# Optimization experiments

Hardware: AMD Instinct MI355X
Metric: run time of the kernel (lower is better)

Reference implementation:

```python
import jax, jax.numpy as jnp
import numpy as np

N_USERS, N_ITEMS, N_TOPICS = 200000, 100000, 100
N_NODES = N_USERS + N_ITEMS + N_TOPICS
N_EDGES = 5000000
DIM = 64
LAYERS = 3
BATCH = 16384


def setup_inputs() -> dict:
    key = jax.random.key(0)
    ks = jax.random.split(key, 8)
    users = jax.random.randint(ks[0], (BATCH,), 0, N_USERS, dtype=jnp.int64 if jax.config.jax_enable_x64 else jnp.int32)
    items = jax.random.randint(ks[1], (BATCH,), 0, N_ITEMS, dtype=jnp.int64 if jax.config.jax_enable_x64 else jnp.int32)
    edge_rows = jax.random.randint(ks[2], (N_EDGES,), 0, N_NODES, dtype=jnp.int32)
    edge_cols = jax.random.randint(ks[3], (N_EDGES,), 0, N_NODES, dtype=jnp.int32)
    # values ~ 1/deg to mimic the symmetric-normalized A_hat of LightGCN
    edge_vals = jax.random.uniform(ks[4], (N_EDGES,), dtype=jnp.float32) / 16.0
    user_emb = 0.1 * jax.random.normal(ks[5], (N_USERS, DIM), dtype=jnp.float32)
    item_emb = 0.1 * jax.random.normal(ks[6], (N_ITEMS, DIM), dtype=jnp.float32)
    topic_emb = 0.1 * jax.random.normal(ks[7], (N_TOPICS, DIM), dtype=jnp.float32)
    return {"users": users, "items": items, "edge_rows": edge_rows,
            "edge_cols": edge_cols, "edge_vals": edge_vals,
            "user_emb": user_emb, "item_emb": item_emb, "topic_emb": topic_emb}


def reference(users, items, edge_rows, edge_cols, edge_vals, user_emb, item_emb, topic_emb):
    n_users = user_emb.shape[0]
    n_nodes = n_users + item_emb.shape[0] + topic_emb.shape[0]
    # E^0 = [users; items; topics]
    h = jnp.concatenate([user_emb, item_emb, topic_emb], axis=0)  # [N, dim]
    acc = h
    for _ in range(LAYERS):
        # sparse A_hat @ h : gather source rows, scale by edge weight, scatter-add to dst
        msgs = edge_vals[:, None] * h[edge_cols]                  # [E, dim]
        h = jax.ops.segment_sum(msgs, edge_rows, num_segments=n_nodes)
        acc = acc + h
    out = acc / (LAYERS + 1)                                      # stack-mean over layers
    u = out[users]                                                # [B, dim]
    it = out[n_users + items]                                     # items offset into node table
    return jnp.sum(u * it, axis=1)                                # [B]
```

## Files before the change

kernel.cpp:

```cpp
#include <hip/hip_runtime.h>
#include <hip/hip_fp16.h>

#define N_USERS  200000
#define N_ITEMS  100000
#define N_TOPICS 100
#define N_NODES  (N_USERS + N_ITEMS + N_TOPICS)
#define DIM      64
#define BSHIFT   9
#define BROWS    (1 << BSHIFT)
#define NBUCKETS ((N_NODES + BROWS - 1) >> BSHIFT)
#define COLMASK  0x7FFFF
#define NB       512
#define NBSHIFT  9
#define M_TOT    (NBUCKETS * NB)
#define SB       256
#define CH       ((M_TOT + SB - 1) / SB)


__global__ void bucket_hist_kernel(const int* __restrict__ rows,
                                   int* __restrict__ partial, int n_edges) {
    __shared__ int h[NBUCKETS];
    for (int i = threadIdx.x; i < NBUCKETS; i += blockDim.x) h[i] = 0;
    __syncthreads();
    int stride = gridDim.x * blockDim.x;
    for (int e = blockIdx.x * blockDim.x + threadIdx.x; e < n_edges; e += stride)
        atomicAdd(&h[((unsigned)rows[e]) >> BSHIFT], 1);
    __syncthreads();
    for (int i = threadIdx.x; i < NBUCKETS; i += blockDim.x)
        partial[blockIdx.x * NBUCKETS + i] = h[i];
}

__device__ __forceinline__ int phys_idx(int L) {
    return (L & (NB - 1)) * NBUCKETS + (L >> NBSHIFT);
}

__global__ void scanB1_kernel(const int* __restrict__ partial,
                              int* __restrict__ psum) {
    __shared__ int s[256];
    int tid = threadIdx.x;
    int c0 = blockIdx.x * CH;
    int c1 = min(M_TOT, c0 + CH);
    int sum = 0;
    for (int L = c0 + tid; L < c1; L += 256) sum += partial[phys_idx(L)];
    s[tid] = sum;
    __syncthreads();
    for (int off = 128; off > 0; off >>= 1) {
        if (tid < off) s[tid] += s[tid + off];
        __syncthreads();
    }
    if (tid == 0) psum[blockIdx.x] = s[0];
}

__global__ void scanB2_kernel(int* __restrict__ psum) {
    __shared__ int s[SB];
    int tid = threadIdx.x;
    s[tid] = psum[tid];
    __syncthreads();
    for (int off = 1; off < SB; off <<= 1) {
        int v = (tid >= off) ? s[tid - off] : 0;
        __syncthreads();
        s[tid] += v;
        __syncthreads();
    }
    psum[tid] = tid ? s[tid - 1] : 0;
}

__global__ void scanB3_kernel(const int* __restrict__ partial,
                              const int* __restrict__ psum,
                              int* __restrict__ offs) {
    __shared__ int tile[256];
    __shared__ int carry;
    int tid = threadIdx.x;
    int c0 = blockIdx.x * CH;
    int c1 = min(M_TOT, c0 + CH);
    if (tid == 0) carry = psum[blockIdx.x];
    __syncthreads();
    for (int base = c0; base < c1; base += 256) {
        int L = base + tid;
        int v = (L < c1) ? partial[phys_idx(L)] : 0;
        tile[tid] = v;
        __syncthreads();
        for (int off = 1; off < 256; off <<= 1) {
            int t = (tid >= off) ? tile[tid - off] : 0;
            __syncthreads();
            tile[tid] += t;
            __syncthreads();
        }
        if (L < c1) offs[L] = carry + tile[tid] - v;
        __syncthreads();
        if (tid == 255) carry += tile[255];
        __syncthreads();
    }
}

__global__ void scatter1_kernel(const int* __restrict__ rows,
                                const int* __restrict__ cols,
                                const float* __restrict__ vals,
                                const int* __restrict__ offs,
                                int2* __restrict__ bkt_buf, int n_edges) {
    __shared__ int lpos[NBUCKETS];
    for (int i = threadIdx.x; i < NBUCKETS; i += blockDim.x)
        lpos[i] = offs[i * NB + blockIdx.x];
    __syncthreads();
    int stride = gridDim.x * blockDim.x;
    for (int e = blockIdx.x * blockDim.x + threadIdx.x; e < n_edges; e += stride) {
        int r = rows[e];
        int b = ((unsigned)r) >> BSHIFT;
        int pos = atomicAdd(&lpos[b], 1);
        int2 p;
        p.x = cols[e] | ((r & (BROWS - 1)) << 19);
        p.y = __float_as_int(vals[e]);
        bkt_buf[pos] = p;
    }
}

__global__ void scatter2_kernel(const int2* __restrict__ bkt_buf,
                                const int* __restrict__ offs,
                                int* __restrict__ row_ptr,
                                int2* __restrict__ csr_cv, int n_edges) {
    __shared__ int lcnt[BROWS];
    __shared__ int lptr[BROWS];
    __shared__ int lfill[BROWS];
    __shared__ int s[256];
    int b = blockIdx.x;
    int t = threadIdx.x;
    int e0 = offs[b * NB];
    int e1 = (b == NBUCKETS - 1) ? n_edges : offs[(b + 1) * NB];
    lcnt[t] = 0;          lcnt[t + 256] = 0;
    lfill[t] = 0;         lfill[t + 256] = 0;
    __syncthreads();
    for (int e = e0 + t; e < e1; e += blockDim.x)
        atomicAdd(&lcnt[((unsigned)bkt_buf[e].x) >> 19], 1);
    __syncthreads();
    s[t] = lcnt[2 * t] + lcnt[2 * t + 1];
    __syncthreads();
    for (int off = 1; off < 256; off <<= 1) {
        int v = (t >= off) ? s[t - off] : 0;
        __syncthreads();
        s[t] += v;
        __syncthreads();
    }
    int base = e0 + (t ? s[t - 1] : 0);
    int rbase = b << BSHIFT;
    int p_even = base;
    int p_odd  = base + lcnt[2 * t];
    lptr[2 * t]     = p_even;
    lptr[2 * t + 1] = p_odd;
    if (rbase + 2 * t     < N_NODES) row_ptr[rbase + 2 * t]     = p_even;
    if (rbase + 2 * t + 1 < N_NODES) row_ptr[rbase + 2 * t + 1] = p_odd;
    if (b == NBUCKETS - 1 && t == 0) row_ptr[N_NODES] = n_edges;
    __syncthreads();
    for (int e = e0 + t; e < e1; e += blockDim.x) {
        int2 p = bkt_buf[e];
        int delta = ((unsigned)p.x) >> 19;
        int pos = lptr[delta] + atomicAdd(&lfill[delta], 1);
        int2 cv;
        cv.x = p.x & COLMASK;
        cv.y = p.y;
        csr_cv[pos] = cv;
    }
}

__global__ void concat_f16_kernel(const float* __restrict__ uemb,
                                  const float* __restrict__ iemb,
                                  const float* __restrict__ temb,
                                  ushort* __restrict__ h0) {
    int g = blockIdx.x * blockDim.x + threadIdx.x;
    long base = (long)g * 4;
    if (base >= (long)N_NODES * DIM) return;
    const float* src;
    long off;
    if (base < (long)N_USERS * DIM)                 { src = uemb; off = base; }
    else if (base < (long)(N_USERS + N_ITEMS) * DIM){ src = iemb; off = base - (long)N_USERS * DIM; }
    else                                            { src = temb; off = base - (long)(N_USERS + N_ITEMS) * DIM; }
    float4 v = *(const float4*)(src + off);
    __half2 a = __floats2half2_rn(v.x, v.y);
    __half2 b = __floats2half2_rn(v.z, v.w);
    uint2 o;
    o.x = *(unsigned*)&a;
    o.y = *(unsigned*)&b;
    ((uint2*)h0)[g] = o;
}

__device__ __forceinline__ float4 fma_mix4(const ushort* __restrict__ h,
                                           int row, int l16, float w,
                                           float4 acc) {
    uint2 r = ((const uint2*)(h + (size_t)row * DIM))[l16];
    __half2 h01 = *(__half2*)&r.x;
    __half2 h23 = *(__half2*)&r.y;
    acc.x = __builtin_fmaf(__half2float(__low2half(h01)),  w, acc.x);
    acc.y = __builtin_fmaf(__half2float(__high2half(h01)), w, acc.y);
    acc.z = __builtin_fmaf(__half2float(__low2half(h23)),  w, acc.z);
    acc.w = __builtin_fmaf(__half2float(__high2half(h23)), w, acc.w);
    return acc;
}

__global__ void spmv_csr_kernel(const int* __restrict__ row_ptr,
                                const int2* __restrict__ csr_cv,
                                const ushort* __restrict__ h_src,
                                ushort* __restrict__ h_dst) {
    int wave = (int)(((long)blockIdx.x * blockDim.x + threadIdx.x) >> 6);
    int lane = threadIdx.x & 63;
    int g    = lane >> 4;
    int l16  = lane & 15;
    int r    = wave * 4 + g;
    int rc   = min(r, N_NODES - 1);
    int p0   = row_ptr[rc];
    int p1   = row_ptr[rc + 1];
    int len  = (r < N_NODES) ? (p1 - p0) : 0;
    int m = max(len, __shfl_xor(len, 16, 64));
    m = max(m, __shfl_xor(m, 32, 64));
    float4 acc = make_float4(0.f, 0.f, 0.f, 0.f);
    for (int off = 0; off < m; off += 8) {
        int2 cv[8];
        #pragma unroll
        for (int j = 0; j < 8; ++j) {
            bool k = (off + j) < len;
            cv[j] = csr_cv[k ? (p0 + off + j) : p0];
            if (!k) cv[j].y = 0;
        }
        #pragma unroll
        for (int j = 0; j < 8; ++j)
            acc = fma_mix4(h_src, cv[j].x, l16, __int_as_float(cv[j].y), acc);
    }
    if (r < N_NODES) {
        __half2 a = __floats2half2_rn(acc.x, acc.y);
        __half2 b = __floats2half2_rn(acc.z, acc.w);
        uint2 o;
        o.x = *(unsigned*)&a;
        o.y = *(unsigned*)&b;
        ((uint2*)(h_dst + (size_t)r * DIM))[l16] = o;
    }
}

__global__ void spmv_batch_kernel(const int* __restrict__ row_ptr,
                                  const int2* __restrict__ csr_cv,
                                  const ushort* __restrict__ h_src,
                                  const int* __restrict__ users,
                                  const int* __restrict__ items,
                                  float* __restrict__ u_acc,
                                  float* __restrict__ it_acc, int B) {
    int wave = (int)(((long)blockIdx.x * blockDim.x + threadIdx.x) >> 6);
    int lane = threadIdx.x & 63;
    int g    = lane >> 4;
    int l16  = lane & 15;
    int s    = wave * 4 + g;
    bool ok  = s < 2 * B;
    int node = 0;
    if (ok) node = (s < B) ? users[s] : (N_USERS + items[s - B]);
    int p0  = row_ptr[node];
    int p1  = row_ptr[node + 1];
    int len = ok ? (p1 - p0) : 0;
    int m = max(len, __shfl_xor(len, 16, 64));
    m = max(m, __shfl_xor(m, 32, 64));
    float4 acc = make_float4(0.f, 0.f, 0.f, 0.f);
    for (int off = 0; off < m; off += 8) {
        int2 cv[8];
        #pragma unroll
        for (int j = 0; j < 8; ++j) {
            bool k = (off + j) < len;
            cv[j] = csr_cv[k ? (p0 + off + j) : p0];
            if (!k) cv[j].y = 0;
        }
        #pragma unroll
        for (int j = 0; j < 8; ++j)
            acc = fma_mix4(h_src, cv[j].x, l16, __int_as_float(cv[j].y), acc);
    }
    if (ok) {
        float* dst = (s < B) ? (u_acc + (size_t)s * DIM)
                             : (it_acc + (size_t)(s - B) * DIM);
        float4* p = (float4*)dst + l16;
        float4 old = *p;
        old.x += acc.x; old.y += acc.y; old.z += acc.z; old.w += acc.w;
        *p = old;
    }
}


__global__ void gather_add_kernel(const ushort* __restrict__ h,
                                  const int* __restrict__ users,
                                  const int* __restrict__ items,
                                  float* __restrict__ u_acc,
                                  float* __restrict__ it_acc,
                                  int B, int first) {
    int gid  = blockIdx.x * blockDim.x + threadIdx.x;
    int b    = gid >> 4;
    int lane = gid & 15;
    if (b >= B) return;
    int u  = users[b];
    int it = N_USERS + items[b];
    uint2 ur = ((const uint2*)(h + (size_t)u  * DIM))[lane];
    uint2 ir = ((const uint2*)(h + (size_t)it * DIM))[lane];
    float2 u01 = __half22float2(*(__half2*)&ur.x);
    float2 u23 = __half22float2(*(__half2*)&ur.y);
    float2 i01 = __half22float2(*(__half2*)&ir.x);
    float2 i23 = __half22float2(*(__half2*)&ir.y);
    float4* up = (float4*)(u_acc  + (size_t)b * DIM) + lane;
    float4* ip = (float4*)(it_acc + (size_t)b * DIM) + lane;
    if (first) {
        *up = make_float4(u01.x, u01.y, u23.x, u23.y);
        *ip = make_float4(i01.x, i01.y, i23.x, i23.y);
    } else {
        float4 a = *up;
        a.x += u01.x; a.y += u01.y; a.z += u23.x; a.w += u23.y;
        *up = a;
        float4 c = *ip;
        c.x += i01.x; c.y += i01.y; c.z += i23.x; c.w += i23.y;
        *ip = c;
    }
}

__global__ void dot_kernel(const float* __restrict__ u_acc,
                           const float* __restrict__ it_acc,
                           float* __restrict__ out, int B) {
    int gid  = blockIdx.x * blockDim.x + threadIdx.x;
    int b    = gid >> 6;
    int lane = gid & 63;
    if (b >= B) return;
    float p = u_acc[(size_t)b * DIM + lane] * it_acc[(size_t)b * DIM + lane];
    #pragma unroll
    for (int off = 32; off > 0; off >>= 1)
        p += __shfl_down(p, off, 64);
    if (lane == 0) out[b] = p * (1.0f / 16.0f);
}

extern "C" void kernel_launch(void* const* d_in, const int* in_sizes, int n_in,
                              void* d_out, int out_size, void* d_ws, size_t ws_size,
                              hipStream_t stream) {
    const int*   users = (const int*)d_in[0];
    const int*   items = (const int*)d_in[1];
    const int*   erows = (const int*)d_in[2];
    const int*   ecols = (const int*)d_in[3];
    const float* evals = (const float*)d_in[4];
    const float* uemb  = (const float*)d_in[5];
    const float* iemb  = (const float*)d_in[6];
    const float* temb  = (const float*)d_in[7];
    float* out = (float*)d_out;

    const int n_edges = in_sizes[2];
    const int B       = in_sizes[0];

    const size_t h2bytes = (((size_t)N_NODES * DIM * 2 + 255) / 256) * 256;
    const size_t abytes  = (size_t)B * DIM * sizeof(float);
    const size_t rpbytes = (((size_t)(N_NODES + 1) * 4 + 255) / 256) * 256;
    const size_t cvbytes = (size_t)n_edges * 8;
    const size_t mbytes  = (((size_t)M_TOT * 4 + 255) / 256) * 256;

    char* ws = (char*)d_ws;
    size_t off = 0;
    ushort* hA      = (ushort*)(ws + off); off += h2bytes;
    ushort* hB      = (ushort*)(ws + off); off += h2bytes;
    float*  u_acc   = (float*) (ws + off); off += abytes;
    float*  it_acc  = (float*) (ws + off); off += abytes;
    int*    row_ptr = (int*)   (ws + off); off += rpbytes;
    int2*   csr_cv  = (int2*)  (ws + off); off += cvbytes;
    int2*   bkt_buf = (int2*)  (ws + off); off += cvbytes;
    int*    partial = (int*)   (ws + off); off += mbytes;
    int*    offs    = (int*)   (ws + off); off += mbytes;
    int*    psum    = (int*)   (ws + off); off += 4096;

    dim3 blk(256);

    bucket_hist_kernel<<<NB, blk, 0, stream>>>(erows, partial, n_edges);
    scanB1_kernel<<<SB, blk, 0, stream>>>(partial, psum);
    scanB2_kernel<<<1,  SB,  0, stream>>>(psum);
    scanB3_kernel<<<SB, blk, 0, stream>>>(partial, psum, offs);
    scatter1_kernel<<<NB, blk, 0, stream>>>(erows, ecols, evals, offs, bkt_buf, n_edges);
    scatter2_kernel<<<NBUCKETS, blk, 0, stream>>>(bkt_buf, offs, row_ptr, csr_cv, n_edges);

    const long n4 = (long)N_NODES * DIM / 4;
    concat_f16_kernel<<<(int)((n4 + 255) / 256), blk, 0, stream>>>(uemb, iemb, temb, hA);

    const int gblocks = (B * 16 + 255) / 256;
    gather_add_kernel<<<gblocks, blk, 0, stream>>>(hA, users, items, u_acc, it_acc, B, 1);

    const int nwaves  = (N_NODES + 3) / 4;
    const int sblocks = (int)(((long)nwaves * 64 + 255) / 256);
    ushort* src = hA;
    ushort* dst = hB;
    for (int l = 0; l < 2; ++l) {
        spmv_csr_kernel<<<sblocks, blk, 0, stream>>>(row_ptr, csr_cv, src, dst);
        gather_add_kernel<<<gblocks, blk, 0, stream>>>(dst, users, items, u_acc, it_acc, B, 0);
        ushort* t = src; src = dst; dst = t;
    }
    const int bwaves  = (2 * B + 3) / 4;
    const int bblocks = (int)(((long)bwaves * 64 + 255) / 256);
    spmv_batch_kernel<<<bblocks, blk, 0, stream>>>(row_ptr, csr_cv, src,
                                                   users, items, u_acc, it_acc, B);

    dot_kernel<<<(B * 64 + 255) / 256, blk, 0, stream>>>(u_acc, it_acc, out, B);
}
```

Before: 602.6 us.

## Vectorize CSR build, fuse scan stages, split bucket SoA, nontemporal SpMV accesses

Histogram and bucket-scatter kernels read edges with 128-bit loads and run with 1024-thread blocks. The middle scan kernel is removed, and each block of the final scan reduces the preceding partial sums itself. The bucket buffer becomes separate key and value arrays. SpMV uses nontemporal loads for edge data and nontemporal stores for outputs to cut cache pollution. The initial accumulator gather reads the fp32 embeddings directly, which also avoids fp16 rounding of layer 0.

```diff
diff --git a/kernel.cpp b/kernel.cpp
--- a/kernel.cpp
+++ b/kernel.cpp
@@ -22,9 +22,20 @@
     __shared__ int h[NBUCKETS];
     for (int i = threadIdx.x; i < NBUCKETS; i += blockDim.x) h[i] = 0;
     __syncthreads();
+    int n4 = n_edges >> 2;
     int stride = gridDim.x * blockDim.x;
-    for (int e = blockIdx.x * blockDim.x + threadIdx.x; e < n_edges; e += stride)
-        atomicAdd(&h[((unsigned)rows[e]) >> BSHIFT], 1);
+    int gid = blockIdx.x * blockDim.x + threadIdx.x;
+    const int4* r4 = (const int4*)rows;
+    for (int e = gid; e < n4; e += stride) {
+        int4 v = r4[e];
+        atomicAdd(&h[((unsigned)v.x) >> BSHIFT], 1);
+        atomicAdd(&h[((unsigned)v.y) >> BSHIFT], 1);
+        atomicAdd(&h[((unsigned)v.z) >> BSHIFT], 1);
+        atomicAdd(&h[((unsigned)v.w) >> BSHIFT], 1);
+    }
+    int tail0 = n4 << 2;
+    if (gid < n_edges - tail0)
+        atomicAdd(&h[((unsigned)rows[tail0 + gid]) >> BSHIFT], 1);
     __syncthreads();
     for (int i = threadIdx.x; i < NBUCKETS; i += blockDim.x)
         partial[blockIdx.x * NBUCKETS + i] = h[i];
@@ -51,30 +62,23 @@
     if (tid == 0) psum[blockIdx.x] = s[0];
 }
 
-__global__ void scanB2_kernel(int* __restrict__ psum) {
-    __shared__ int s[SB];
-    int tid = threadIdx.x;
-    s[tid] = psum[tid];
-    __syncthreads();
-    for (int off = 1; off < SB; off <<= 1) {
-        int v = (tid >= off) ? s[tid - off] : 0;
-        __syncthreads();
-        s[tid] += v;
-        __syncthreads();
-    }
-    psum[tid] = tid ? s[tid - 1] : 0;
-}
-
 __global__ void scanB3_kernel(const int* __restrict__ partial,
                               const int* __restrict__ psum,
                               int* __restrict__ offs) {
+    __shared__ int s[SB];
     __shared__ int tile[256];
     __shared__ int carry;
     int tid = threadIdx.x;
+    s[tid] = (tid < blockIdx.x) ? psum[tid] : 0;
+    __syncthreads();
+    for (int off = 128; off > 0; off >>= 1) {
+        if (tid < off) s[tid] += s[tid + off];
+        __syncthreads();
+    }
+    if (tid == 0) carry = s[0];
+    __syncthreads();
     int c0 = blockIdx.x * CH;
     int c1 = min(M_TOT, c0 + CH);
-    if (tid == 0) carry = psum[blockIdx.x];
-    __syncthreads();
     for (int base = c0; base < c1; base += 256) {
         int L = base + tid;
         int v = (L < c1) ? partial[phys_idx(L)] : 0;
@@ -97,24 +101,46 @@
                                 const int* __restrict__ cols,
                                 const float* __restrict__ vals,
                                 const int* __restrict__ offs,
-                                int2* __restrict__ bkt_buf, int n_edges) {
+                                int* __restrict__ bkt_key,
+                                float* __restrict__ bkt_val, int n_edges) {
     __shared__ int lpos[NBUCKETS];
     for (int i = threadIdx.x; i < NBUCKETS; i += blockDim.x)
         lpos[i] = offs[i * NB + blockIdx.x];
     __syncthreads();
+    int n4 = n_edges >> 2;
     int stride = gridDim.x * blockDim.x;
-    for (int e = blockIdx.x * blockDim.x + threadIdx.x; e < n_edges; e += stride) {
-        int r = rows[e];
-        int b = ((unsigned)r) >> BSHIFT;
+    int gid = blockIdx.x * blockDim.x + threadIdx.x;
+    const int4*   r4 = (const int4*)rows;
+    const int4*   c4 = (const int4*)cols;
+    const float4* v4 = (const float4*)vals;
+    for (int e = gid; e < n4; e += stride) {
+        int4 r = r4[e];
+        int4 c = c4[e];
+        float4 v = v4[e];
+        #pragma unroll
+        for (int j = 0; j < 4; ++j) {
+            int rr = (j == 0) ? r.x : (j == 1) ? r.y : (j == 2) ? r.z : r.w;
+            int cc = (j == 0) ? c.x : (j == 1) ? c.y : (j == 2) ? c.z : c.w;
+            float vv = (j == 0) ? v.x : (j == 1) ? v.y : (j == 2) ? v.z : v.w;
+            int b = ((unsigned)rr) >> BSHIFT;
+            int pos = atomicAdd(&lpos[b], 1);
+            bkt_key[pos] = cc | ((rr & (BROWS - 1)) << 19);
+            bkt_val[pos] = vv;
+        }
+    }
+    int tail0 = n4 << 2;
+    if (gid < n_edges - tail0) {
+        int e = tail0 + gid;
+        int rr = rows[e];
+        int b = ((unsigned)rr) >> BSHIFT;
         int pos = atomicAdd(&lpos[b], 1);
-        int2 p;
-        p.x = cols[e] | ((r & (BROWS - 1)) << 19);
-        p.y = __float_as_int(vals[e]);
-        bkt_buf[pos] = p;
-    }
-}
-
-__global__ void scatter2_kernel(const int2* __restrict__ bkt_buf,
+        bkt_key[pos] = cols[e] | ((rr & (BROWS - 1)) << 19);
+        bkt_val[pos] = vals[e];
+    }
+}
+
+__global__ void scatter2_kernel(const int* __restrict__ bkt_key,
+                                const float* __restrict__ bkt_val,
                                 const int* __restrict__ offs,
                                 int* __restrict__ row_ptr,
                                 int2* __restrict__ csr_cv, int n_edges) {
@@ -126,37 +152,40 @@
     int t = threadIdx.x;
     int e0 = offs[b * NB];
     int e1 = (b == NBUCKETS - 1) ? n_edges : offs[(b + 1) * NB];
-    lcnt[t] = 0;          lcnt[t + 256] = 0;
-    lfill[t] = 0;         lfill[t + 256] = 0;
+    for (int i = t; i < BROWS; i += blockDim.x) { lcnt[i] = 0; lfill[i] = 0; }
     __syncthreads();
     for (int e = e0 + t; e < e1; e += blockDim.x)
-        atomicAdd(&lcnt[((unsigned)bkt_buf[e].x) >> 19], 1);
-    __syncthreads();
-    s[t] = lcnt[2 * t] + lcnt[2 * t + 1];
+        atomicAdd(&lcnt[((unsigned)bkt_key[e]) >> 19], 1);
+    __syncthreads();
+    if (t < 256) s[t] = lcnt[2 * t] + lcnt[2 * t + 1];
     __syncthreads();
     for (int off = 1; off < 256; off <<= 1) {
-        int v = (t >= off) ? s[t - off] : 0;
-        __syncthreads();
-        s[t] += v;
-        __syncthreads();
-    }
-    int base = e0 + (t ? s[t - 1] : 0);
-    int rbase = b << BSHIFT;
-    int p_even = base;
-    int p_odd  = base + lcnt[2 * t];
-    lptr[2 * t]     = p_even;
-    lptr[2 * t + 1] = p_odd;
-    if (rbase + 2 * t     < N_NODES) row_ptr[rbase + 2 * t]     = p_even;
-    if (rbase + 2 * t + 1 < N_NODES) row_ptr[rbase + 2 * t + 1] = p_odd;
+        int v = 0;
+        if (t < 256 && t >= off) v = s[t - off];
+        __syncthreads();
+        if (t < 256) s[t] += v;
+        __syncthreads();
+    }
+    if (t < 256) {
+        int base = e0 + (t ? s[t - 1] : 0);
+        int rbase = b << BSHIFT;
+        int p_even = base;
+        int p_odd  = base + lcnt[2 * t];
+        lptr[2 * t]     = p_even;
+        lptr[2 * t + 1] = p_odd;
+        if (rbase + 2 * t     < N_NODES) row_ptr[rbase + 2 * t]     = p_even;
+        if (rbase + 2 * t + 1 < N_NODES) row_ptr[rbase + 2 * t + 1] = p_odd;
+    }
     if (b == NBUCKETS - 1 && t == 0) row_ptr[N_NODES] = n_edges;
     __syncthreads();
     for (int e = e0 + t; e < e1; e += blockDim.x) {
-        int2 p = bkt_buf[e];
-        int delta = ((unsigned)p.x) >> 19;
+        int k = bkt_key[e];
+        float v = bkt_val[e];
+        int delta = ((unsigned)k) >> 19;
         int pos = lptr[delta] + atomicAdd(&lfill[delta], 1);
         int2 cv;
-        cv.x = p.x & COLMASK;
-        cv.y = p.y;
+        cv.x = k & COLMASK;
+        cv.y = __float_as_int(v);
         csr_cv[pos] = cv;
     }
 }
@@ -180,6 +209,15 @@
     o.x = *(unsigned*)&a;
     o.y = *(unsigned*)&b;
     ((uint2*)h0)[g] = o;
+}
+
+__device__ __forceinline__ int2 ld_nt_int2(const int2* __restrict__ p) {
+    unsigned long long v =
+        __builtin_nontemporal_load((const unsigned long long*)p);
+    int2 r;
+    r.x = (int)(unsigned)v;
+    r.y = (int)(v >> 32);
+    return r;
 }
 
 __device__ __forceinline__ float4 fma_mix4(const ushort* __restrict__ h,
@@ -216,7 +254,7 @@
         #pragma unroll
         for (int j = 0; j < 8; ++j) {
             bool k = (off + j) < len;
-            cv[j] = csr_cv[k ? (p0 + off + j) : p0];
+            cv[j] = ld_nt_int2(csr_cv + (k ? (p0 + off + j) : p0));
             if (!k) cv[j].y = 0;
         }
         #pragma unroll
@@ -226,10 +264,11 @@
     if (r < N_NODES) {
         __half2 a = __floats2half2_rn(acc.x, acc.y);
         __half2 b = __floats2half2_rn(acc.z, acc.w);
-        uint2 o;
-        o.x = *(unsigned*)&a;
-        o.y = *(unsigned*)&b;
-        ((uint2*)(h_dst + (size_t)r * DIM))[l16] = o;
+        unsigned long long o =
+            (unsigned long long)(*(unsigned*)&a) |
+            ((unsigned long long)(*(unsigned*)&b) << 32);
+        __builtin_nontemporal_store(
+            o, (unsigned long long*)((uint2*)(h_dst + (size_t)r * DIM) + l16));
     }
 }
 
@@ -259,7 +298,7 @@
         #pragma unroll
         for (int j = 0; j < 8; ++j) {
             bool k = (off + j) < len;
-            cv[j] = csr_cv[k ? (p0 + off + j) : p0];
+            cv[j] = ld_nt_int2(csr_cv + (k ? (p0 + off + j) : p0));
             if (!k) cv[j].y = 0;
         }
         #pragma unroll
@@ -277,12 +316,29 @@
 }
 
 
+__global__ void gather_init_kernel(const float* __restrict__ uemb,
+                                   const float* __restrict__ iemb,
+                                   const int* __restrict__ users,
+                                   const int* __restrict__ items,
+                                   float* __restrict__ u_acc,
+                                   float* __restrict__ it_acc, int B) {
+    int gid  = blockIdx.x * blockDim.x + threadIdx.x;
+    int b    = gid >> 4;
+    int lane = gid & 15;
+    if (b >= B) return;
+    int u  = users[b];
+    int it = items[b];
+    float4 uv = ((const float4*)(uemb + (size_t)u  * DIM))[lane];
+    float4 iv = ((const float4*)(iemb + (size_t)it * DIM))[lane];
+    ((float4*)(u_acc  + (size_t)b * DIM))[lane] = uv;
+    ((float4*)(it_acc + (size_t)b * DIM))[lane] = iv;
+}
+
 __global__ void gather_add_kernel(const ushort* __restrict__ h,
                                   const int* __restrict__ users,
                                   const int* __restrict__ items,
                                   float* __restrict__ u_acc,
-                                  float* __restrict__ it_acc,
-                                  int B, int first) {
+                                  float* __restrict__ it_acc, int B) {
     int gid  = blockIdx.x * blockDim.x + threadIdx.x;
     int b    = gid >> 4;
     int lane = gid & 15;
@@ -297,17 +353,12 @@
     float2 i23 = __half22float2(*(__half2*)&ir.y);
     float4* up = (float4*)(u_acc  + (size_t)b * DIM) + lane;
     float4* ip = (float4*)(it_acc + (size_t)b * DIM) + lane;
-    if (first) {
-        *up = make_float4(u01.x, u01.y, u23.x, u23.y);
-        *ip = make_float4(i01.x, i01.y, i23.x, i23.y);
-    } else {
-        float4 a = *up;
-        a.x += u01.x; a.y += u01.y; a.z += u23.x; a.w += u23.y;
-        *up = a;
-        float4 c = *ip;
-        c.x += i01.x; c.y += i01.y; c.z += i23.x; c.w += i23.y;
-        *ip = c;
-    }
+    float4 a = *up;
+    a.x += u01.x; a.y += u01.y; a.z += u23.x; a.w += u23.y;
+    *up = a;
+    float4 c = *ip;
+    c.x += i01.x; c.y += i01.y; c.z += i23.x; c.w += i23.y;
+    *ip = c;
 }
 
 __global__ void dot_kernel(const float* __restrict__ u_acc,
@@ -344,6 +395,7 @@
     const size_t abytes  = (size_t)B * DIM * sizeof(float);
     const size_t rpbytes = (((size_t)(N_NODES + 1) * 4 + 255) / 256) * 256;
     const size_t cvbytes = (size_t)n_edges * 8;
+    const size_t kbytes  = (size_t)n_edges * 4;
     const size_t mbytes  = (((size_t)M_TOT * 4 + 255) / 256) * 256;
 
     char* ws = (char*)d_ws;
@@ -354,25 +406,29 @@
     float*  it_acc  = (float*) (ws + off); off += abytes;
     int*    row_ptr = (int*)   (ws + off); off += rpbytes;
     int2*   csr_cv  = (int2*)  (ws + off); off += cvbytes;
-    int2*   bkt_buf = (int2*)  (ws + off); off += cvbytes;
+    int*    bkt_key = (int*)   (ws + off); off += kbytes;
+    float*  bkt_val = (float*) (ws + off); off += kbytes;
     int*    partial = (int*)   (ws + off); off += mbytes;
     int*    offs    = (int*)   (ws + off); off += mbytes;
     int*    psum    = (int*)   (ws + off); off += 4096;
 
     dim3 blk(256);
-
-    bucket_hist_kernel<<<NB, blk, 0, stream>>>(erows, partial, n_edges);
+    dim3 blk1k(1024);
+
+    bucket_hist_kernel<<<NB, blk1k, 0, stream>>>(erows, partial, n_edges);
     scanB1_kernel<<<SB, blk, 0, stream>>>(partial, psum);
-    scanB2_kernel<<<1,  SB,  0, stream>>>(psum);
     scanB3_kernel<<<SB, blk, 0, stream>>>(partial, psum, offs);
-    scatter1_kernel<<<NB, blk, 0, stream>>>(erows, ecols, evals, offs, bkt_buf, n_edges);
-    scatter2_kernel<<<NBUCKETS, blk, 0, stream>>>(bkt_buf, offs, row_ptr, csr_cv, n_edges);
+    scatter1_kernel<<<NB, blk1k, 0, stream>>>(erows, ecols, evals, offs,
+                                              bkt_key, bkt_val, n_edges);
+    scatter2_kernel<<<NBUCKETS, blk1k, 0, stream>>>(bkt_key, bkt_val, offs,
+                                                    row_ptr, csr_cv, n_edges);
 
     const long n4 = (long)N_NODES * DIM / 4;
     concat_f16_kernel<<<(int)((n4 + 255) / 256), blk, 0, stream>>>(uemb, iemb, temb, hA);
 
     const int gblocks = (B * 16 + 255) / 256;
-    gather_add_kernel<<<gblocks, blk, 0, stream>>>(hA, users, items, u_acc, it_acc, B, 1);
+    gather_init_kernel<<<gblocks, blk, 0, stream>>>(uemb, iemb, users, items,
+                                                    u_acc, it_acc, B);
 
     const int nwaves  = (N_NODES + 3) / 4;
     const int sblocks = (int)(((long)nwaves * 64 + 255) / 256);
@@ -380,7 +436,8 @@
     ushort* dst = hB;
     for (int l = 0; l < 2; ++l) {
         spmv_csr_kernel<<<sblocks, blk, 0, stream>>>(row_ptr, csr_cv, src, dst);
-        gather_add_kernel<<<gblocks, blk, 0, stream>>>(dst, users, items, u_acc, it_acc, B, 0);
+        gather_add_kernel<<<gblocks, blk, 0, stream>>>(dst, users, items,
+                                                       u_acc, it_acc, B);
         ushort* t = src; src = dst; dst = t;
     }
     const int bwaves  = (2 * B + 3) / 4;
```

Measured after the change: 678.8 us. 12.7% more time.
